# Kernel tuning notes

Measured on AMD Instinct MI355X. Metric: run time of the kernel, lower is better.

## Reference

```python
import jax, jax.numpy as jnp
import numpy as np

EMBED = 1024
HEADS = 16
HEAD_DIM = EMBED // HEADS


def setup_inputs() -> dict:
    key = jax.random.key(0)
    ks = jax.random.split(key, 8)
    N, L = 2, 2048
    values = jax.random.normal(ks[0], (N, L, EMBED), dtype=jnp.float32)
    keys_ = jax.random.normal(ks[1], (N, L, EMBED), dtype=jnp.float32)
    query = jax.random.normal(ks[2], (N, L, EMBED), dtype=jnp.float32)
    mask = jnp.ones((N, 1, 1, L), dtype=jnp.int32)
    s = 1.0 / np.sqrt(EMBED)
    W_q = jax.random.normal(ks[3], (EMBED, EMBED), dtype=jnp.float32) * s
    W_k = jax.random.normal(ks[4], (EMBED, EMBED), dtype=jnp.float32) * s
    W_v = jax.random.normal(ks[5], (EMBED, EMBED), dtype=jnp.float32) * s
    W_o = jax.random.normal(ks[6], (EMBED, EMBED), dtype=jnp.float32) * s
    b_o = jax.random.normal(ks[7], (EMBED,), dtype=jnp.float32) * 0.01
    return {"values": values, "keys": keys_, "query": query, "mask": mask,
            "W_q": W_q, "W_k": W_k, "W_v": W_v, "W_o": W_o, "b_o": b_o}


def reference(values, keys, query, mask, W_q, W_k, W_v, W_o, b_o):
    N, Lq, _ = query.shape
    Lk = keys.shape[1]
    # projections (torch Linear: x @ W.T); reshape to (N, H, L, Dh)
    q = (query @ W_q.T).reshape(N, Lq, HEADS, HEAD_DIM).transpose(0, 2, 1, 3)
    k = (keys @ W_k.T).reshape(N, Lk, HEADS, HEAD_DIM).transpose(0, 2, 1, 3)
    v = (values @ W_v.T).reshape(N, Lk, HEADS, HEAD_DIM).transpose(0, 2, 1, 3)
    energy = jnp.einsum('bhqd,bhkd->bhqk', q, k) / jnp.sqrt(jnp.float32(HEAD_DIM))
    energy = jnp.where(mask == 0, jnp.float32(-1e20), energy)
    attn = jax.nn.softmax(energy, axis=-1)
    out = jnp.einsum('bhqk,bhkd->bhqd', attn, v)
    out = out.transpose(0, 2, 1, 3).reshape(N, Lq, EMBED)
    return out @ W_o.T + b_o
```

## Files before the change

kernel.cpp:

```cpp
#include <hip/hip_runtime.h>
#include <cstddef>
#include <cstdint>

#define SEQ    2048
#define NBATCH 2

typedef unsigned short u16;
typedef unsigned int   u32;
typedef __attribute__((ext_vector_type(8))) short bf16x8;
typedef __attribute__((ext_vector_type(4))) float f32x4;

#if __has_builtin(__builtin_amdgcn_exp2f)
#define EXP2F(x) __builtin_amdgcn_exp2f(x)
#else
#define EXP2F(x) exp2f(x)
#endif

__device__ __forceinline__ u32 fbits(float x) { union { float f; u32 u; } c; c.f = x; return c.u; }
__device__ __forceinline__ u16 f2bf(float x) { return (u16)((fbits(x) + 0x8000u) >> 16); }
__device__ __forceinline__ u32 pack2bf(float lo, float hi) {
    return __builtin_amdgcn_perm(fbits(hi) + 0x8000u, fbits(lo) + 0x8000u, 0x07060302u);
}

__global__ __launch_bounds__(256)
void cast3(const float* __restrict__ a, const float* __restrict__ b, const float* __restrict__ c,
           u16* __restrict__ oa, u16* __restrict__ ob, u16* __restrict__ oc, int n4)
{
    const float* s; u16* d;
    if (blockIdx.y == 0)      { s = a; d = oa; }
    else if (blockIdx.y == 1) { s = b; d = ob; }
    else                      { s = c; d = oc; }
    int i = blockIdx.x * 256 + threadIdx.x;
    if (i >= n4) return;
    float4 v = ((const float4*)s)[i];
    uint2 r; r.x = pack2bf(v.x, v.y); r.y = pack2bf(v.z, v.w);
    ((uint2*)d)[i] = r;
}

__global__ __launch_bounds__(256)
void cast4(const float* __restrict__ a, const float* __restrict__ b,
           const float* __restrict__ c, const float* __restrict__ e,
           u16* __restrict__ oa, u16* __restrict__ ob, u16* __restrict__ oc, u16* __restrict__ oe,
           int n4)
{
    const float* s; u16* d;
    if (blockIdx.y == 0)      { s = a; d = oa; }
    else if (blockIdx.y == 1) { s = b; d = ob; }
    else if (blockIdx.y == 2) { s = c; d = oc; }
    else                      { s = e; d = oe; }
    int i = blockIdx.x * 256 + threadIdx.x;
    if (i >= n4) return;
    float4 v = ((const float4*)s)[i];
    uint2 r; r.x = pack2bf(v.x, v.y); r.y = pack2bf(v.z, v.w);
    ((uint2*)d)[i] = r;
}

__device__ __forceinline__
void gemm_body(const u16* __restrict__ X, const u16* __restrict__ W,
               void* __restrict__ Yv, const float* __restrict__ bias, const int layout)
{
    __shared__ u16 smem[2 * 128 * 72];
    u16* As = smem;
    u16* Bs = smem + 128 * 72;

    const int tid  = threadIdx.x;
    const int wave = tid >> 6;
    const int lane = tid & 63;
    const int lm   = lane & 15;
    const int quad = lane >> 4;
    const int m0 = blockIdx.x * 128;
    const int n0 = blockIdx.y * 128;
    const int wr = (wave & 1) * 64;
    const int wc = (wave >> 1) * 64;

    const int srow = tid >> 1;
    const int scol = (tid & 1) * 32;
    const u16* xg = X + (size_t)(m0 + srow) * 1024 + scol;
    const u16* wg = W + (size_t)(n0 + srow) * 1024 + scol;

    bf16x8 pa[4], pb[4];
    #pragma unroll
    for (int p = 0; p < 4; ++p) {
        pa[p] = *(const bf16x8*)(xg + p * 8);
        pb[p] = *(const bf16x8*)(wg + p * 8);
    }

    f32x4 acc[4][4] = {};

    for (int k0 = 0; k0 < 1024; k0 += 64) {
        __syncthreads();
        #pragma unroll
        for (int p = 0; p < 4; ++p) {
            *(bf16x8*)&As[srow * 72 + scol + p * 8] = pa[p];
            *(bf16x8*)&Bs[srow * 72 + scol + p * 8] = pb[p];
        }
        __syncthreads();
        if (k0 + 64 < 1024) {
            #pragma unroll
            for (int p = 0; p < 4; ++p) {
                pa[p] = *(const bf16x8*)(xg + k0 + 64 + p * 8);
                pb[p] = *(const bf16x8*)(wg + k0 + 64 + p * 8);
            }
        }
        #pragma unroll
        for (int kk = 0; kk < 64; kk += 32) {
            bf16x8 af[4], bf[4];
            #pragma unroll
            for (int t = 0; t < 4; ++t) {
                af[t] = *(const bf16x8*)&As[(wr + t * 16 + lm) * 72 + kk + quad * 8];
                bf[t] = *(const bf16x8*)&Bs[(wc + t * 16 + lm) * 72 + kk + quad * 8];
            }
            #pragma unroll
            for (int i = 0; i < 4; ++i)
                #pragma unroll
                for (int j = 0; j < 4; ++j)
                    acc[i][j] = __builtin_amdgcn_mfma_f32_16x16x32_bf16(af[i], bf[j], acc[i][j], 0, 0, 0);
        }
    }

    if (layout == 3) {
        float* Y = (float*)Yv;
        #pragma unroll
        for (int i = 0; i < 4; ++i)
            #pragma unroll
            for (int j = 0; j < 4; ++j) {
                const int C = n0 + wc + j * 16 + lm;
                const float bv = bias[C];
                #pragma unroll
                for (int r = 0; r < 4; ++r) {
                    const int R = m0 + wr + i * 16 + quad * 4 + r;
                    Y[(size_t)R * 1024 + C] = acc[i][j][r] + bv;
                }
            }
    } else if (layout == 0) {
        u16* Y = (u16*)Yv;
        #pragma unroll
        for (int i = 0; i < 4; ++i)
            #pragma unroll
            for (int j = 0; j < 4; ++j) {
                const int C = n0 + wc + j * 16 + lm;
                #pragma unroll
                for (int r = 0; r < 4; ++r) {
                    const int R = m0 + wr + i * 16 + quad * 4 + r;
                    Y[(size_t)R * 1024 + C] = f2bf(acc[i][j][r]);
                }
            }
    } else {
        __syncthreads();
        u16* T = smem;
        #pragma unroll
        for (int i = 0; i < 4; ++i)
            #pragma unroll
            for (int j = 0; j < 4; ++j) {
                const int col = wc + j * 16 + lm;
                const int row = wr + i * 16 + quad * 4;
                uint2 v;
                v.x = pack2bf(acc[i][j][0], acc[i][j][1]);
                v.y = pack2bf(acc[i][j][2], acc[i][j][3]);
                *(uint2*)&T[col * 132 + row] = v;
            }
        __syncthreads();
        const int dp = tid >> 1, half = (tid & 1) * 64;
        const int nn = m0 >> 11, l0 = m0 & 2047;
        const int C = n0 + dp, h = C >> 6, d = C & 63;
        u16* Y = (u16*)Yv;
        const size_t base = (((size_t)nn * 16 + h) * 64 + d) * SEQ + l0 + half;
        #pragma unroll
        for (int p = 0; p < 8; ++p) {
            bf16x8 v = *(const bf16x8*)&T[dp * 132 + half + p * 8];
            *(bf16x8*)(Y + base + p * 8) = v;
        }
    }
}

__global__ __launch_bounds__(256, 2)
void gemm_qkv(const u16* __restrict__ xq, const u16* __restrict__ xk, const u16* __restrict__ xv,
              const u16* __restrict__ wq, const u16* __restrict__ wk, const u16* __restrict__ wv,
              u16* __restrict__ qb, u16* __restrict__ kb, u16* __restrict__ vt)
{
    if (blockIdx.z == 0)      gemm_body(xq, wq, qb, nullptr, 0);
    else if (blockIdx.z == 1) gemm_body(xk, wk, kb, nullptr, 0);
    else                      gemm_body(xv, wv, vt, nullptr, 2);
}

__global__ __launch_bounds__(256, 2)
void gemm_out(const u16* __restrict__ X, const u16* __restrict__ W,
              float* __restrict__ Y, const float* __restrict__ bias)
{
    gemm_body(X, W, Y, bias, 3);
}

__global__ __launch_bounds__(256, 2)
void flash_attn_bf16(const u16* __restrict__ Qb, const u16* __restrict__ Kb,
                     const u16* __restrict__ VT, const int* __restrict__ mask,
                     u16* __restrict__ O)
{
    __shared__ u16 Ks[64 * 72];
    __shared__ u16 Vts[64 * 72];
    __shared__ u16 Ps[4][32 * 72];

    const int tid  = threadIdx.x;
    const int wave = tid >> 6;
    const int lane = tid & 63;
    const int lm   = lane & 15;
    const int quad = lane >> 4;
    const int h = blockIdx.y, n = blockIdx.z;
    const int wq = blockIdx.x * 128 + wave * 32;

    const u16* Qh = Qb + ((size_t)n * SEQ) * 1024 + h * 64;
    const u16* Kh = Kb + ((size_t)n * SEQ) * 1024 + h * 64;
    const u16* Vh = VT + (((size_t)n * 16 + h) * 64) * SEQ;
    const int* mk = mask + (size_t)n * SEQ;
    u16* Pw = &Ps[wave][0];

    bf16x8 qf[2][2];
    #pragma unroll
    for (int t = 0; t < 2; ++t)
        #pragma unroll
        for (int s = 0; s < 2; ++s)
            qf[t][s] = *(const bf16x8*)(Qh + (size_t)(wq + t * 16 + lm) * 1024 + s * 32 + quad * 8);

    f32x4 o_acc[2][4] = {};
    float l_i[2][4] = {};

    const int srow = lane;
    const int d0   = wave * 16;

    bf16x8 ka, kb2, va, vb;
    ka  = *(const bf16x8*)(Kh + (size_t)srow * 1024 + d0);
    kb2 = *(const bf16x8*)(Kh + (size_t)srow * 1024 + d0 + 8);
    va  = *(const bf16x8*)(Vh + (size_t)srow * SEQ + d0);
    vb  = *(const bf16x8*)(Vh + (size_t)srow * SEQ + d0 + 8);

    const float cs = 0.125f * 1.44269504f;

    for (int c0 = 0; c0 < SEQ; c0 += 64) {
        __syncthreads();
        *(bf16x8*)&Ks[srow * 72 + d0]      = ka;
        *(bf16x8*)&Ks[srow * 72 + d0 + 8]  = kb2;
        *(bf16x8*)&Vts[srow * 72 + d0]     = va;
        *(bf16x8*)&Vts[srow * 72 + d0 + 8] = vb;
        __syncthreads();

        if (c0 + 64 < SEQ) {
            ka  = *(const bf16x8*)(Kh + (size_t)(c0 + 64 + srow) * 1024 + d0);
            kb2 = *(const bf16x8*)(Kh + (size_t)(c0 + 64 + srow) * 1024 + d0 + 8);
            va  = *(const bf16x8*)(Vh + (size_t)srow * SEQ + c0 + 64 + d0);
            vb  = *(const bf16x8*)(Vh + (size_t)srow * SEQ + c0 + 64 + d0 + 8);
        }

        f32x4 s[2][4] = {};
        #pragma unroll
        for (int nt = 0; nt < 4; ++nt) {
            bf16x8 kf0 = *(const bf16x8*)&Ks[(nt * 16 + lm) * 72 + quad * 8];
            bf16x8 kf1 = *(const bf16x8*)&Ks[(nt * 16 + lm) * 72 + 32 + quad * 8];
            #pragma unroll
            for (int t = 0; t < 2; ++t) {
                s[t][nt] = __builtin_amdgcn_mfma_f32_16x16x32_bf16(qf[t][0], kf0, s[t][nt], 0, 0, 0);
                s[t][nt] = __builtin_amdgcn_mfma_f32_16x16x32_bf16(qf[t][1], kf1, s[t][nt], 0, 0, 0);
            }
        }

        int msk[4];
        #pragma unroll
        for (int nt = 0; nt < 4; ++nt) msk[nt] = mk[c0 + nt * 16 + lm];
        #pragma unroll
        for (int t = 0; t < 2; ++t)
            #pragma unroll
            for (int nt = 0; nt < 4; ++nt)
                #pragma unroll
                for (int r = 0; r < 4; ++r) {
                    float e = EXP2F(s[t][nt][r] * cs);
                    e = msk[nt] ? e : 0.0f;
                    s[t][nt][r] = e;
                    l_i[t][r] += e;
                }

        #pragma unroll
        for (int t = 0; t < 2; ++t)
            #pragma unroll
            for (int nt = 0; nt < 4; ++nt)
                #pragma unroll
                for (int r = 0; r < 4; ++r)
                    Pw[(t * 16 + quad * 4 + r) * 72 + nt * 16 + lm] = f2bf(s[t][nt][r]);

        #pragma unroll
        for (int ks = 0; ks < 2; ++ks) {
            bf16x8 pf[2];
            #pragma unroll
            for (int t = 0; t < 2; ++t)
                pf[t] = *(const bf16x8*)&Pw[(t * 16 + lm) * 72 + ks * 32 + quad * 8];
            #pragma unroll
            for (int dt = 0; dt < 4; ++dt) {
                bf16x8 vf = *(const bf16x8*)&Vts[(dt * 16 + lm) * 72 + ks * 32 + quad * 8];
                #pragma unroll
                for (int t = 0; t < 2; ++t)
                    o_acc[t][dt] = __builtin_amdgcn_mfma_f32_16x16x32_bf16(pf[t], vf, o_acc[t][dt], 0, 0, 0);
            }
        }
    }

    #pragma unroll
    for (int t = 0; t < 2; ++t)
        #pragma unroll
        for (int r = 0; r < 4; ++r) {
            float v = l_i[t][r];
            #pragma unroll
            for (int off = 1; off < 16; off <<= 1) v += __shfl_xor(v, off);
            l_i[t][r] = 1.0f / v;
        }
    #pragma unroll
    for (int t = 0; t < 2; ++t)
        #pragma unroll
        for (int dt = 0; dt < 4; ++dt)
            #pragma unroll
            for (int r = 0; r < 4; ++r) {
                const int ql = wq + t * 16 + quad * 4 + r;
                const int col = h * 64 + dt * 16 + lm;
                O[((size_t)n * SEQ + ql) * 1024 + col] = f2bf(o_acc[t][dt][r] * l_i[t][r]);
            }
}

extern "C" void kernel_launch(void* const* d_in, const int* in_sizes, int n_in,
                              void* d_out, int out_size, void* d_ws, size_t ws_size,
                              hipStream_t stream)
{
    const float* values = (const float*)d_in[0];
    const float* keys   = (const float*)d_in[1];
    const float* query  = (const float*)d_in[2];
    const int*   mask   = (const int*)d_in[3];
    const float* W_q    = (const float*)d_in[4];
    const float* W_k    = (const float*)d_in[5];
    const float* W_v    = (const float*)d_in[6];
    const float* W_o    = (const float*)d_in[7];
    const float* b_o    = (const float*)d_in[8];

    const size_t NTOK = (size_t)NBATCH * SEQ * 1024;
    const size_t WSZ  = 1024 * 1024;
    u16* p = (u16*)d_ws;
    u16* qb    = p; p += NTOK;
    u16* kb    = p; p += NTOK;
    u16* vt    = p; p += NTOK;
    u16* attnb = p; p += NTOK;
    u16* xq    = p; p += NTOK;
    u16* xk    = p; p += NTOK;
    u16* xv    = p; p += NTOK;
    u16* wqb   = p; p += WSZ;
    u16* wkb   = p; p += WSZ;
    u16* wvb   = p; p += WSZ;
    u16* wob   = p; p += WSZ;

    cast3<<<dim3(4096, 3), 256, 0, stream>>>(query, keys, values, xq, xk, xv, (int)(NTOK / 4));
    cast4<<<dim3(1024, 4), 256, 0, stream>>>(W_q, W_k, W_v, W_o, wqb, wkb, wvb, wob, (int)(WSZ / 4));

    gemm_qkv<<<dim3(32, 8, 3), 256, 0, stream>>>(xq, xk, xv, wqb, wkb, wvb, qb, kb, vt);

    flash_attn_bf16<<<dim3(16, 16, 2), 256, 0, stream>>>(qb, kb, vt, mask, attnb);

    gemm_out<<<dim3(32, 8), 256, 0, stream>>>(attnb, wob, (float*)d_out, b_o);
}
```

Baseline: 236.4 us.

## Split-K output projection with reduce kernel and widen attention KV tile

The output projection GEMM is split along K into two halves, which doubles the block count from 256 to 512 so the GPU's compute units are better filled. The two fp32 partial results go into reused workspace buffers, and a separate reduction kernel sums them and adds the bias. The flash attention kernel also moves from 64 to 128 keys per tile, which halves the number of loop iterations and barriers. In exchange it uses more shared memory and registers for a larger score array, which may lower occupancy. The split-K path also adds extra global traffic and one more kernel launch.

After: 236.9 us. About the same (+0.2%).

```diff
diff --git a/kernel.cpp b/kernel.cpp
--- a/kernel.cpp
+++ b/kernel.cpp
@@ -57,7 +57,8 @@
 
 __device__ __forceinline__
 void gemm_body(const u16* __restrict__ X, const u16* __restrict__ W,
-               void* __restrict__ Yv, const float* __restrict__ bias, const int layout)
+               void* __restrict__ Yv, const float* __restrict__ bias, const int layout,
+               const int kbeg, const int kend)
 {
     __shared__ u16 smem[2 * 128 * 72];
     u16* As = smem;
@@ -81,13 +82,13 @@
     bf16x8 pa[4], pb[4];
     #pragma unroll
     for (int p = 0; p < 4; ++p) {
-        pa[p] = *(const bf16x8*)(xg + p * 8);
-        pb[p] = *(const bf16x8*)(wg + p * 8);
+        pa[p] = *(const bf16x8*)(xg + kbeg + p * 8);
+        pb[p] = *(const bf16x8*)(wg + kbeg + p * 8);
     }
 
     f32x4 acc[4][4] = {};
 
-    for (int k0 = 0; k0 < 1024; k0 += 64) {
+    for (int k0 = kbeg; k0 < kend; k0 += 64) {
         __syncthreads();
         #pragma unroll
         for (int p = 0; p < 4; ++p) {
@@ -95,7 +96,7 @@
             *(bf16x8*)&Bs[srow * 72 + scol + p * 8] = pb[p];
         }
         __syncthreads();
-        if (k0 + 64 < 1024) {
+        if (k0 + 64 < kend) {
             #pragma unroll
             for (int p = 0; p < 4; ++p) {
                 pa[p] = *(const bf16x8*)(xg + k0 + 64 + p * 8);
@@ -125,7 +126,7 @@
             #pragma unroll
             for (int j = 0; j < 4; ++j) {
                 const int C = n0 + wc + j * 16 + lm;
-                const float bv = bias[C];
+                const float bv = bias ? bias[C] : 0.0f;
                 #pragma unroll
                 for (int r = 0; r < 4; ++r) {
                     const int R = m0 + wr + i * 16 + quad * 4 + r;
@@ -178,16 +179,31 @@
               const u16* __restrict__ wq, const u16* __restrict__ wk, const u16* __restrict__ wv,
               u16* __restrict__ qb, u16* __restrict__ kb, u16* __restrict__ vt)
 {
-    if (blockIdx.z == 0)      gemm_body(xq, wq, qb, nullptr, 0);
-    else if (blockIdx.z == 1) gemm_body(xk, wk, kb, nullptr, 0);
-    else                      gemm_body(xv, wv, vt, nullptr, 2);
+    if (blockIdx.z == 0)      gemm_body(xq, wq, qb, nullptr, 0, 0, 1024);
+    else if (blockIdx.z == 1) gemm_body(xk, wk, kb, nullptr, 0, 0, 1024);
+    else                      gemm_body(xv, wv, vt, nullptr, 2, 0, 1024);
 }
 
 __global__ __launch_bounds__(256, 2)
-void gemm_out(const u16* __restrict__ X, const u16* __restrict__ W,
-              float* __restrict__ Y, const float* __restrict__ bias)
-{
-    gemm_body(X, W, Y, bias, 3);
+void gemm_out_split(const u16* __restrict__ X, const u16* __restrict__ W,
+                    float* __restrict__ p0, float* __restrict__ p1)
+{
+    if (blockIdx.z == 0) gemm_body(X, W, p0, nullptr, 3, 0, 512);
+    else                 gemm_body(X, W, p1, nullptr, 3, 512, 1024);
+}
+
+__global__ __launch_bounds__(256)
+void reduce_bias(const float* __restrict__ p0, const float* __restrict__ p1,
+                 const float* __restrict__ bias, float* __restrict__ out)
+{
+    const int i = blockIdx.x * 256 + threadIdx.x;
+    float4 a = ((const float4*)p0)[i];
+    float4 b = ((const float4*)p1)[i];
+    float4 c = ((const float4*)bias)[i & 255];
+    float4 o;
+    o.x = a.x + b.x + c.x; o.y = a.y + b.y + c.y;
+    o.z = a.z + b.z + c.z; o.w = a.w + b.w + c.w;
+    ((float4*)out)[i] = o;
 }
 
 __global__ __launch_bounds__(256, 2)
@@ -195,8 +211,8 @@
                      const u16* __restrict__ VT, const int* __restrict__ mask,
                      u16* __restrict__ O)
 {
-    __shared__ u16 Ks[64 * 72];
-    __shared__ u16 Vts[64 * 72];
+    __shared__ u16 Ks[128 * 72];
+    __shared__ u16 Vts[64 * 136];
     __shared__ u16 Ps[4][32 * 72];
 
     const int tid  = threadIdx.x;
@@ -223,35 +239,38 @@
     f32x4 o_acc[2][4] = {};
     float l_i[2][4] = {};
 
-    const int srow = lane;
-    const int d0   = wave * 16;
-
-    bf16x8 ka, kb2, va, vb;
-    ka  = *(const bf16x8*)(Kh + (size_t)srow * 1024 + d0);
-    kb2 = *(const bf16x8*)(Kh + (size_t)srow * 1024 + d0 + 8);
-    va  = *(const bf16x8*)(Vh + (size_t)srow * SEQ + d0);
-    vb  = *(const bf16x8*)(Vh + (size_t)srow * SEQ + d0 + 8);
+    const int kr = tid >> 1, kc = (tid & 1) * 32;
+    const int vr = tid >> 2, vc = (tid & 3) * 32;
+
+    bf16x8 ka[4], va[4];
+    #pragma unroll
+    for (int p = 0; p < 4; ++p) {
+        ka[p] = *(const bf16x8*)(Kh + (size_t)kr * 1024 + kc + p * 8);
+        va[p] = *(const bf16x8*)(Vh + (size_t)vr * SEQ + vc + p * 8);
+    }
 
     const float cs = 0.125f * 1.44269504f;
 
-    for (int c0 = 0; c0 < SEQ; c0 += 64) {
-        __syncthreads();
-        *(bf16x8*)&Ks[srow * 72 + d0]      = ka;
-        *(bf16x8*)&Ks[srow * 72 + d0 + 8]  = kb2;
-        *(bf16x8*)&Vts[srow * 72 + d0]     = va;
-        *(bf16x8*)&Vts[srow * 72 + d0 + 8] = vb;
-        __syncthreads();
-
-        if (c0 + 64 < SEQ) {
-            ka  = *(const bf16x8*)(Kh + (size_t)(c0 + 64 + srow) * 1024 + d0);
-            kb2 = *(const bf16x8*)(Kh + (size_t)(c0 + 64 + srow) * 1024 + d0 + 8);
-            va  = *(const bf16x8*)(Vh + (size_t)srow * SEQ + c0 + 64 + d0);
-            vb  = *(const bf16x8*)(Vh + (size_t)srow * SEQ + c0 + 64 + d0 + 8);
-        }
-
-        f32x4 s[2][4] = {};
-        #pragma unroll
-        for (int nt = 0; nt < 4; ++nt) {
+    for (int c0 = 0; c0 < SEQ; c0 += 128) {
+        __syncthreads();
+        #pragma unroll
+        for (int p = 0; p < 4; ++p) {
+            *(bf16x8*)&Ks[kr * 72 + kc + p * 8]   = ka[p];
+            *(bf16x8*)&Vts[vr * 136 + vc + p * 8] = va[p];
+        }
+        __syncthreads();
+
+        if (c0 + 128 < SEQ) {
+            #pragma unroll
+            for (int p = 0; p < 4; ++p) {
+                ka[p] = *(const bf16x8*)(Kh + (size_t)(c0 + 128 + kr) * 1024 + kc + p * 8);
+                va[p] = *(const bf16x8*)(Vh + (size_t)vr * SEQ + c0 + 128 + vc + p * 8);
+            }
+        }
+
+        f32x4 s[2][8] = {};
+        #pragma unroll
+        for (int nt = 0; nt < 8; ++nt) {
             bf16x8 kf0 = *(const bf16x8*)&Ks[(nt * 16 + lm) * 72 + quad * 8];
             bf16x8 kf1 = *(const bf16x8*)&Ks[(nt * 16 + lm) * 72 + 32 + quad * 8];
             #pragma unroll
@@ -261,13 +280,13 @@
             }
         }
 
-        int msk[4];
-        #pragma unroll
-        for (int nt = 0; nt < 4; ++nt) msk[nt] = mk[c0 + nt * 16 + lm];
+        int msk[8];
+        #pragma unroll
+        for (int nt = 0; nt < 8; ++nt) msk[nt] = mk[c0 + nt * 16 + lm];
         #pragma unroll
         for (int t = 0; t < 2; ++t)
             #pragma unroll
-            for (int nt = 0; nt < 4; ++nt)
+            for (int nt = 0; nt < 8; ++nt)
                 #pragma unroll
                 for (int r = 0; r < 4; ++r) {
                     float e = EXP2F(s[t][nt][r] * cs);
@@ -277,25 +296,29 @@
                 }
 
         #pragma unroll
-        for (int t = 0; t < 2; ++t)
-            #pragma unroll
-            for (int nt = 0; nt < 4; ++nt)
-                #pragma unroll
-                for (int r = 0; r < 4; ++r)
-                    Pw[(t * 16 + quad * 4 + r) * 72 + nt * 16 + lm] = f2bf(s[t][nt][r]);
-
-        #pragma unroll
-        for (int ks = 0; ks < 2; ++ks) {
-            bf16x8 pf[2];
+        for (int half = 0; half < 2; ++half) {
             #pragma unroll
             for (int t = 0; t < 2; ++t)
-                pf[t] = *(const bf16x8*)&Pw[(t * 16 + lm) * 72 + ks * 32 + quad * 8];
-            #pragma unroll
-            for (int dt = 0; dt < 4; ++dt) {
-                bf16x8 vf = *(const bf16x8*)&Vts[(dt * 16 + lm) * 72 + ks * 32 + quad * 8];
+                #pragma unroll
+                for (int ntl = 0; ntl < 4; ++ntl)
+                    #pragma unroll
+                    for (int r = 0; r < 4; ++r)
+                        Pw[(t * 16 + quad * 4 + r) * 72 + ntl * 16 + lm] =
+                            f2bf(s[t][half * 4 + ntl][r]);
+
+            #pragma unroll
+            for (int ksl = 0; ksl < 2; ++ksl) {
+                bf16x8 pf[2];
                 #pragma unroll
                 for (int t = 0; t < 2; ++t)
-                    o_acc[t][dt] = __builtin_amdgcn_mfma_f32_16x16x32_bf16(pf[t], vf, o_acc[t][dt], 0, 0, 0);
+                    pf[t] = *(const bf16x8*)&Pw[(t * 16 + lm) * 72 + ksl * 32 + quad * 8];
+                #pragma unroll
+                for (int dt = 0; dt < 4; ++dt) {
+                    bf16x8 vf = *(const bf16x8*)&Vts[(dt * 16 + lm) * 136 + half * 64 + ksl * 32 + quad * 8];
+                    #pragma unroll
+                    for (int t = 0; t < 2; ++t)
+                        o_acc[t][dt] = __builtin_amdgcn_mfma_f32_16x16x32_bf16(pf[t], vf, o_acc[t][dt], 0, 0, 0);
+                }
             }
         }
     }
@@ -341,14 +364,16 @@
     u16* qb    = p; p += NTOK;
     u16* kb    = p; p += NTOK;
     u16* vt    = p; p += NTOK;
-    u16* attnb = p; p += NTOK;
     u16* xq    = p; p += NTOK;
     u16* xk    = p; p += NTOK;
     u16* xv    = p; p += NTOK;
+    u16* attnb = p; p += NTOK;
     u16* wqb   = p; p += WSZ;
     u16* wkb   = p; p += WSZ;
     u16* wvb   = p; p += WSZ;
     u16* wob   = p; p += WSZ;
+    float* part0 = (float*)qb;
+    float* part1 = (float*)vt;
 
     cast3<<<dim3(4096, 3), 256, 0, stream>>>(query, keys, values, xq, xk, xv, (int)(NTOK / 4));
     cast4<<<dim3(1024, 4), 256, 0, stream>>>(W_q, W_k, W_v, W_o, wqb, wkb, wvb, wob, (int)(WSZ / 4));
@@ -357,5 +382,6 @@
 
     flash_attn_bf16<<<dim3(16, 16, 2), 256, 0, stream>>>(qb, kb, vt, mask, attnb);
 
-    gemm_out<<<dim3(32, 8), 256, 0, stream>>>(attnb, wob, (float*)d_out, b_o);
-}
+    gemm_out_split<<<dim3(32, 8, 2), 256, 0, stream>>>(attnb, wob, part0, part1);
+    reduce_bias<<<4096, 256, 0, stream>>>(part0, part1, b_o, (float*)d_out);
+}
```
